# Kernel optimization log

Measured on AMD Instinct MI355X. Metric: run time of the kernel, lower is better.

The kernel has to match this reference:

```python
import jax, jax.numpy as jnp
import numpy as np

NUM_HEADS = 16  # matches init_kwargs; used only for the softmax scale


def setup_inputs() -> dict:
    key = jax.random.key(0)
    ks = jax.random.split(key, 6)
    B, S, H = 2, 4096, 2048
    W_STD = 0.02  # keep pre-softmax logits in a sane range
    return {
        "hidden_states": jax.random.normal(ks[0], (B, S, H), dtype=jnp.float32),
        "freqs_angle": jax.random.uniform(ks[1], (H // 2,), dtype=jnp.float32),
        "wq": jax.random.normal(ks[2], (H, H), dtype=jnp.float32) * W_STD,
        "wk": jax.random.normal(ks[3], (H, H), dtype=jnp.float32) * W_STD,
        "wv": jax.random.normal(ks[4], (H, H), dtype=jnp.float32) * W_STD,
        "wo": jax.random.normal(ks[5], (H, H), dtype=jnp.float32) * W_STD,
        "num_heads": NUM_HEADS,
    }


def _apply_rotary(x, cos, sin):
    # x: [B,S,H]; split full hidden dim into (real, imag) halves of size d=H//2,
    # complex-multiply by exp(i*theta) (theta shape [d], broadcast over B,S),
    # then emit torch.view_as_real's INTERLEAVED layout [re0, im0, re1, im1, ...].
    d = x.shape[-1] // 2
    xr, xi = x[..., :d], x[..., d:]
    out_r = xr * cos - xi * sin
    out_i = xr * sin + xi * cos
    return jnp.stack([out_r, out_i], axis=-1).reshape(x.shape)  # [B,S,2d]


def reference(hidden_states, freqs_angle, wq, wk, wv, wo, num_heads):
    H = hidden_states.shape[-1]
    scale = 1.0 / float(np.sqrt(H // num_heads))

    q = jnp.einsum("bsh,oh->bso", hidden_states, wq)
    k = jnp.einsum("bsh,oh->bso", hidden_states, wk)
    v = jnp.einsum("bsh,oh->bso", hidden_states, wv)

    cos, sin = jnp.cos(freqs_angle), jnp.sin(freqs_angle)
    q_rot = _apply_rotary(q, cos, sin)
    k_rot = _apply_rotary(k, cos, sin)

    # full-hidden-dim attention (module never reshapes into heads)
    scores = jnp.einsum("bqh,bkh->bqk", q_rot, k_rot) * scale  # [B,S,S]
    probs = jax.nn.softmax(scores, axis=-1)
    out = jnp.einsum("bqk,bkh->bqh", probs, v)
    return jnp.einsum("bsh,oh->bso", out, wo)
```

## Files before the change

### kernel.cpp

```cpp
#include <hip/hip_runtime.h>
#include <hip/hip_fp16.h>


typedef _Float16 half8 __attribute__((ext_vector_type(8)));
typedef _Float16 half4v __attribute__((ext_vector_type(4)));
typedef float f32x4 __attribute__((ext_vector_type(4)));

using gas_t = const __attribute__((address_space(1))) void;
using las_t = __attribute__((address_space(3))) void;
#define GL2LDS16(g, l) __builtin_amdgcn_global_load_lds((gas_t*)(g), (las_t*)(l), 16, 0, 0)

#define BAR() __builtin_amdgcn_s_barrier()
#define VMW(N) asm volatile("s_waitcnt vmcnt(" #N ")" ::: "memory")


#define FRAGS(BUF, KS, QC)                                                        \
  half8 af[8], bf[2];                                                             \
  _Pragma("unroll") for (int mi = 0; mi < 8; ++mi)                                \
      af[mi] = *(const half8*)&lds[(BUF)*32768 + (KS)*8192 + aoff + mi*512];      \
  _Pragma("unroll") for (int ni = 0; ni < 2; ++ni)                                \
      bf[ni] = *(const half8*)&lds[(BUF)*32768 + 16384 + (KS)*8192 + boff + (QC)*1024 + ni*512];

#define MFMA8x2(QC)                                                               \
  __builtin_amdgcn_s_setprio(1);                                                  \
  _Pragma("unroll") for (int mi = 0; mi < 8; ++mi) {                              \
    acc[mi][(QC)*2+0] = __builtin_amdgcn_mfma_f32_16x16x32_f16(af[mi], bf[0], acc[mi][(QC)*2+0], 0, 0, 0); \
    acc[mi][(QC)*2+1] = __builtin_amdgcn_mfma_f32_16x16x32_f16(af[mi], bf[1], acc[mi][(QC)*2+1], 0, 0, 0); \
  }                                                                               \
  __builtin_amdgcn_s_setprio(0);

#define STAGE(GP, LD, RB, KT, KS, BUFI, ISB)                                      \
  {                                                                               \
    const _Float16* _s = (GP) + (size_t)((RB) + srow) * (LD) + (KT) + (KS)*32 + scl*8; \
    _Float16* _d = lds + (BUFI)*32768 + (ISB)*16384 + (KS)*8192 + wv*512 + lane*8;     \
    GL2LDS16(_s, _d);                                                             \
    GL2LDS16(_s + (size_t)128*(LD), _d + 4096);                                   \
  }

template <typename OutT>
__global__ __launch_bounds__(512, 2) void gemm256(
    const _Float16* __restrict__ A, const _Float16* __restrict__ B,
    OutT* __restrict__ C, int K, int lda, int ldb, int ldc,
    size_t saz, size_t sbz, size_t scz) {
  extern __shared__ __align__(16) _Float16 lds[];

  const int tid = threadIdx.x;
  const int lane = tid & 63;
  const int wv = tid >> 6;
  const int wr = wv >> 2;
  const int wcol = wv & 3;
  const int r16 = lane & 15, kq = lane >> 4;
  const int chk = kq ^ ((r16 >> 1) & 3);
  const int aoff = (wr * 128 + r16) * 32 + chk * 8;
  const int boff = (wcol * 64 + r16) * 32 + chk * 8;
  const int srow = (wv << 4) + (lane >> 2);
  const int scl = (lane & 3) ^ ((lane >> 3) & 3);

  const int gx = gridDim.x, gy = gridDim.y;
  const int nwg = gx * gy * (int)gridDim.z;
  const int flat = blockIdx.x + gx * (blockIdx.y + gy * blockIdx.z);
  const int swz = (flat & 7) * (nwg >> 3) + (flat >> 3);
  const int tn = swz % gx;
  const int rem = swz / gx;
  const int tm = rem % gy;
  const int bz = rem / gy;
  const _Float16* Ab = A + (size_t)bz * saz;
  const _Float16* Bb = B + (size_t)bz * sbz;
  OutT* Cb = C + (size_t)bz * scz;
  const int mBase = tm * 256, nBase = tn * 256;

  f32x4 acc[8][4] = {};

  STAGE(Ab, lda, mBase, 0, 0, 0, 0);
  STAGE(Bb, ldb, nBase, 0, 0, 0, 1);
  STAGE(Ab, lda, mBase, 0, 1, 0, 0);
  STAGE(Bb, ldb, nBase, 0, 1, 0, 1);
  STAGE(Ab, lda, mBase, 64, 0, 1, 0);
  STAGE(Bb, ldb, nBase, 64, 0, 1, 1);
  VMW(4);
  BAR();

  const int NIT = K >> 7;
  for (int it = 0; it < NIT - 1; ++it) {
    const int kt1 = it * 128 + 64, kt2 = it * 128 + 128, kt3 = it * 128 + 192;
    { FRAGS(0,0,0); STAGE(Ab, lda, mBase, kt1, 1, 1, 0); BAR(); MFMA8x2(0); BAR(); }
    { FRAGS(0,0,1); STAGE(Bb, ldb, nBase, kt1, 1, 1, 1); BAR(); MFMA8x2(1); VMW(8); BAR(); }
    { FRAGS(0,1,0); STAGE(Ab, lda, mBase, kt2, 0, 0, 0); BAR(); MFMA8x2(0); BAR(); }
    { FRAGS(0,1,1); STAGE(Bb, ldb, nBase, kt2, 0, 0, 1); BAR(); MFMA8x2(1); VMW(8); BAR(); }
    { FRAGS(1,0,0); STAGE(Ab, lda, mBase, kt2, 1, 0, 0); BAR(); MFMA8x2(0); BAR(); }
    { FRAGS(1,0,1); STAGE(Bb, ldb, nBase, kt2, 1, 0, 1); BAR(); MFMA8x2(1); VMW(8); BAR(); }
    { FRAGS(1,1,0); STAGE(Ab, lda, mBase, kt3, 0, 1, 0); BAR(); MFMA8x2(0); BAR(); }
    { FRAGS(1,1,1); STAGE(Bb, ldb, nBase, kt3, 0, 1, 1); BAR(); MFMA8x2(1); VMW(8); BAR(); }
  }
  const int ktL = K - 64;
  { FRAGS(0,0,0); STAGE(Ab, lda, mBase, ktL, 1, 1, 0); BAR(); MFMA8x2(0); BAR(); }
  { FRAGS(0,0,1); STAGE(Bb, ldb, nBase, ktL, 1, 1, 1); BAR(); MFMA8x2(1); VMW(8); BAR(); }
  { FRAGS(0,1,0); BAR(); MFMA8x2(0); BAR(); }
  { FRAGS(0,1,1); BAR(); MFMA8x2(1); VMW(4); BAR(); }
  { FRAGS(1,0,0); BAR(); MFMA8x2(0); BAR(); }
  { FRAGS(1,0,1); BAR(); MFMA8x2(1); VMW(0); BAR(); }
  { FRAGS(1,1,0); BAR(); MFMA8x2(0); BAR(); }
  { FRAGS(1,1,1); BAR(); MFMA8x2(1); }

  const size_t crow0 = (size_t)mBase + wr * 128 + kq * 4;
  const size_t ccol = (size_t)nBase + wcol * 64 + r16;
#pragma unroll
  for (int mi = 0; mi < 8; ++mi)
#pragma unroll
    for (int n = 0; n < 4; ++n)
#pragma unroll
      for (int r = 0; r < 4; ++r)
        Cb[(crow0 + mi * 16 + r) * (size_t)ldc + ccol + n * 16] = (OutT)acc[mi][n][r];
}

__global__ __launch_bounds__(256) void prep(
    const float* __restrict__ hid, const float* __restrict__ ang,
    const float* __restrict__ wq, const float* __restrict__ wk,
    const float* __restrict__ wv, const float* __restrict__ wo,
    _Float16* __restrict__ Xh, _Float16* __restrict__ WqR,
    _Float16* __restrict__ WkR, _Float16* __restrict__ Wvh,
    _Float16* __restrict__ Woh) {
  const int z = blockIdx.z;
  const int start = blockIdx.x * 256 + threadIdx.x;
  const int stride = gridDim.x * 256;
  if (z <= 1) {
    const float* w = z ? wk : wq;
    _Float16* o = z ? WkR : WqR;
    const float sc = z ? 1.0f : 0.08838834764831845f;
    for (int u = start; u < 1024 * 512; u += stride) {
      const int i = u >> 9;
      const int c = (u & 511) << 2;
      const float a = ang[i];
      const float cv = cosf(a) * sc, sv = sinf(a) * sc;
      f32x4 ar = *(const f32x4*)&w[(size_t)i * 2048 + c];
      f32x4 br = *(const f32x4*)&w[(size_t)(i + 1024) * 2048 + c];
      half4v r0, r1;
#pragma unroll
      for (int j = 0; j < 4; ++j) {
        r0[j] = (_Float16)(ar[j] * cv - br[j] * sv);
        r1[j] = (_Float16)(ar[j] * sv + br[j] * cv);
      }
      *(half4v*)&o[(size_t)(2 * i) * 2048 + c] = r0;
      *(half4v*)&o[(size_t)(2 * i + 1) * 2048 + c] = r1;
    }
  } else if (z <= 3) {
    const float* w = (z == 2) ? wv : wo;
    _Float16* o = (z == 2) ? Wvh : Woh;
    for (int u = start; u < 2048 * 512; u += stride) {
      const int c = u << 2;
      f32x4 a = *(const f32x4*)&w[c];
      half4v r;
#pragma unroll
      for (int j = 0; j < 4; ++j) r[j] = (_Float16)a[j];
      *(half4v*)&o[c] = r;
    }
  } else {
    for (int u = start; u < (2 * 4096 * 2048) / 4; u += stride) {
      const int c = u << 2;
      f32x4 a = *(const f32x4*)&hid[c];
      half4v r;
#pragma unroll
      for (int j = 0; j < 4; ++j) r[j] = (_Float16)a[j];
      *(half4v*)&Xh[c] = r;
    }
  }
}

__global__ __launch_bounds__(256) void softmax_rows(_Float16* __restrict__ Sm) {
  _Float16* p = Sm + (size_t)blockIdx.x * 4096;
  const int tid = threadIdx.x;
  const int lane = tid & 63, wave = tid >> 6;
  __shared__ float red[8];

  half8 v0 = *(const half8*)&p[tid * 16];
  half8 v1 = *(const half8*)&p[tid * 16 + 8];
  float x[16];
#pragma unroll
  for (int j = 0; j < 8; ++j) { x[j] = (float)v0[j]; x[8 + j] = (float)v1[j]; }

  float m = x[0];
#pragma unroll
  for (int j = 1; j < 16; ++j) m = fmaxf(m, x[j]);
#pragma unroll
  for (int msk = 32; msk >= 1; msk >>= 1) m = fmaxf(m, __shfl_xor(m, msk));
  if (lane == 0) red[wave] = m;
  __syncthreads();
  m = fmaxf(fmaxf(red[0], red[1]), fmaxf(red[2], red[3]));

  float s = 0.f;
#pragma unroll
  for (int j = 0; j < 16; ++j) { x[j] = __expf(x[j] - m); s += x[j]; }
#pragma unroll
  for (int msk = 32; msk >= 1; msk >>= 1) s += __shfl_xor(s, msk);
  if (lane == 0) red[4 + wave] = s;
  __syncthreads();
  s = red[4] + red[5] + red[6] + red[7];
  const float inv = 1.0f / s;

#pragma unroll
  for (int j = 0; j < 8; ++j) {
    v0[j] = (_Float16)(x[j] * inv);
    v1[j] = (_Float16)(x[8 + j] * inv);
  }
  *(half8*)&p[tid * 16] = v0;
  *(half8*)&p[tid * 16 + 8] = v1;
}

extern "C" void kernel_launch(void* const* d_in, const int* in_sizes, int n_in,
                              void* d_out, int out_size, void* d_ws, size_t ws_size,
                              hipStream_t stream) {
  (void)in_sizes; (void)n_in; (void)out_size; (void)ws_size;
  const float* hid = (const float*)d_in[0];
  const float* ang = (const float*)d_in[1];
  const float* wq  = (const float*)d_in[2];
  const float* wk  = (const float*)d_in[3];
  const float* wv  = (const float*)d_in[4];
  const float* wo  = (const float*)d_in[5];
  float* out = (float*)d_out;

  _Float16* ws = (_Float16*)d_ws;
  const size_t EX = 2ull * 4096 * 2048;
  const size_t EH = 2048ull * 2048;
  _Float16* Xh  = ws;
  _Float16* AO  = ws;
  _Float16* Q   = ws + EX;
  _Float16* Kh  = ws + 2 * EX;
  _Float16* Vt  = ws + 3 * EX;
  _Float16* WqR = ws + 4 * EX;
  _Float16* WkR = WqR + EH;
  _Float16* Wvh = WkR + EH;
  _Float16* Woh = Wvh + EH;
  _Float16* Sm  = Woh + EH;

  (void)hipFuncSetAttribute((const void*)&gemm256<_Float16>,
                            hipFuncAttributeMaxDynamicSharedMemorySize, 131072);
  (void)hipFuncSetAttribute((const void*)&gemm256<float>,
                            hipFuncAttributeMaxDynamicSharedMemorySize, 131072);

  prep<<<dim3(2048, 1, 5), 256, 0, stream>>>(hid, ang, wq, wk, wv, wo, Xh, WqR, WkR, Wvh, Woh);

  gemm256<_Float16><<<dim3(8, 32, 2), 512, 131072, stream>>>(
      Xh, WqR, Q, 2048, 2048, 2048, 2048, 0, EH, EX);

  gemm256<_Float16><<<dim3(16, 8, 2), 512, 131072, stream>>>(
      Wvh, Xh, Vt, 2048, 2048, 2048, 4096, 0, (size_t)4096 * 2048, (size_t)2048 * 4096);

  gemm256<_Float16><<<dim3(16, 16, 2), 512, 131072, stream>>>(
      Q, Kh, Sm, 2048, 2048, 2048, 4096, (size_t)4096 * 2048, (size_t)4096 * 2048,
      (size_t)4096 * 4096);

  softmax_rows<<<8192, 256, 0, stream>>>(Sm);

  gemm256<_Float16><<<dim3(8, 16, 2), 512, 131072, stream>>>(
      Sm, Vt, AO, 4096, 4096, 4096, 2048, (size_t)4096 * 4096, (size_t)2048 * 4096,
      (size_t)4096 * 2048);

  gemm256<float><<<dim3(8, 32, 1), 512, 131072, stream>>>(
      AO, Woh, out, 2048, 2048, 2048, 2048, 0, 0, 0);
}
```

Before: 712.1 us.

## Double-buffer MFMA register fragments to overlap LDS reads with matrix math

```diff
diff --git a/kernel.cpp b/kernel.cpp
--- a/kernel.cpp
+++ b/kernel.cpp
@@ -14,18 +14,19 @@
 #define VMW(N) asm volatile("s_waitcnt vmcnt(" #N ")" ::: "memory")
 
 
-#define FRAGS(BUF, KS, QC)                                                        \
-  half8 af[8], bf[2];                                                             \
+#define LDA8(DST, BUF, KS)                                                        \
   _Pragma("unroll") for (int mi = 0; mi < 8; ++mi)                                \
-      af[mi] = *(const half8*)&lds[(BUF)*32768 + (KS)*8192 + aoff + mi*512];      \
+      DST[mi] = *(const half8*)&lds[(BUF)*32768 + (KS)*8192 + aoff + mi*512];
+
+#define LDB2(DST, BUF, KS, QC)                                                    \
   _Pragma("unroll") for (int ni = 0; ni < 2; ++ni)                                \
-      bf[ni] = *(const half8*)&lds[(BUF)*32768 + 16384 + (KS)*8192 + boff + (QC)*1024 + ni*512];
-
-#define MFMA8x2(QC)                                                               \
+      DST[ni] = *(const half8*)&lds[(BUF)*32768 + 16384 + (KS)*8192 + boff + (QC)*1024 + ni*512];
+
+#define MFMA8x2(AF, BF, QC)                                                       \
   __builtin_amdgcn_s_setprio(1);                                                  \
   _Pragma("unroll") for (int mi = 0; mi < 8; ++mi) {                              \
-    acc[mi][(QC)*2+0] = __builtin_amdgcn_mfma_f32_16x16x32_f16(af[mi], bf[0], acc[mi][(QC)*2+0], 0, 0, 0); \
-    acc[mi][(QC)*2+1] = __builtin_amdgcn_mfma_f32_16x16x32_f16(af[mi], bf[1], acc[mi][(QC)*2+1], 0, 0, 0); \
+    acc[mi][(QC)*2+0] = __builtin_amdgcn_mfma_f32_16x16x32_f16(AF[mi], BF[0], acc[mi][(QC)*2+0], 0, 0, 0); \
+    acc[mi][(QC)*2+1] = __builtin_amdgcn_mfma_f32_16x16x32_f16(AF[mi], BF[1], acc[mi][(QC)*2+1], 0, 0, 0); \
   }                                                                               \
   __builtin_amdgcn_s_setprio(0);
 
@@ -70,6 +71,9 @@
   const int mBase = tm * 256, nBase = tn * 256;
 
   f32x4 acc[8][4] = {};
+  half8 afA[8], afB[8];
+  half8 bfA0[2], bfA1[2];
+  half8 bfB0[2], bfB1[2];
 
   STAGE(Ab, lda, mBase, 0, 0, 0, 0);
   STAGE(Bb, ldb, nBase, 0, 0, 0, 1);
@@ -79,28 +83,30 @@
   STAGE(Bb, ldb, nBase, 64, 0, 1, 1);
   VMW(4);
   BAR();
+  LDA8(afA, 0, 0);
+  LDB2(bfA0, 0, 0, 0);
 
   const int NIT = K >> 7;
   for (int it = 0; it < NIT - 1; ++it) {
     const int kt1 = it * 128 + 64, kt2 = it * 128 + 128, kt3 = it * 128 + 192;
-    { FRAGS(0,0,0); STAGE(Ab, lda, mBase, kt1, 1, 1, 0); BAR(); MFMA8x2(0); BAR(); }
-    { FRAGS(0,0,1); STAGE(Bb, ldb, nBase, kt1, 1, 1, 1); BAR(); MFMA8x2(1); VMW(8); BAR(); }
-    { FRAGS(0,1,0); STAGE(Ab, lda, mBase, kt2, 0, 0, 0); BAR(); MFMA8x2(0); BAR(); }
-    { FRAGS(0,1,1); STAGE(Bb, ldb, nBase, kt2, 0, 0, 1); BAR(); MFMA8x2(1); VMW(8); BAR(); }
-    { FRAGS(1,0,0); STAGE(Ab, lda, mBase, kt2, 1, 0, 0); BAR(); MFMA8x2(0); BAR(); }
-    { FRAGS(1,0,1); STAGE(Bb, ldb, nBase, kt2, 1, 0, 1); BAR(); MFMA8x2(1); VMW(8); BAR(); }
-    { FRAGS(1,1,0); STAGE(Ab, lda, mBase, kt3, 0, 1, 0); BAR(); MFMA8x2(0); BAR(); }
-    { FRAGS(1,1,1); STAGE(Bb, ldb, nBase, kt3, 0, 1, 1); BAR(); MFMA8x2(1); VMW(8); BAR(); }
+    { STAGE(Ab, lda, mBase, kt1, 1, 1, 0); BAR(); LDB2(bfA1, 0, 0, 1);                    MFMA8x2(afA, bfA0, 0); VMW(6); BAR(); }
+    { STAGE(Bb, ldb, nBase, kt1, 1, 1, 1); BAR(); LDA8(afB, 0, 1); LDB2(bfB0, 0, 1, 0);   MFMA8x2(afA, bfA1, 1);         BAR(); }
+    { STAGE(Ab, lda, mBase, kt2, 0, 0, 0); BAR(); LDB2(bfB1, 0, 1, 1);                    MFMA8x2(afB, bfB0, 0); VMW(6); BAR(); }
+    { STAGE(Bb, ldb, nBase, kt2, 0, 0, 1); BAR(); LDA8(afA, 1, 0); LDB2(bfA0, 1, 0, 0);   MFMA8x2(afB, bfB1, 1);         BAR(); }
+    { STAGE(Ab, lda, mBase, kt2, 1, 0, 0); BAR(); LDB2(bfA1, 1, 0, 1);                    MFMA8x2(afA, bfA0, 0); VMW(6); BAR(); }
+    { STAGE(Bb, ldb, nBase, kt2, 1, 0, 1); BAR(); LDA8(afB, 1, 1); LDB2(bfB0, 1, 1, 0);   MFMA8x2(afA, bfA1, 1);         BAR(); }
+    { STAGE(Ab, lda, mBase, kt3, 0, 1, 0); BAR(); LDB2(bfB1, 1, 1, 1);                    MFMA8x2(afB, bfB0, 0); VMW(6); BAR(); }
+    { STAGE(Bb, ldb, nBase, kt3, 0, 1, 1); BAR(); LDA8(afA, 0, 0); LDB2(bfA0, 0, 0, 0);   MFMA8x2(afB, bfB1, 1);         BAR(); }
   }
   const int ktL = K - 64;
-  { FRAGS(0,0,0); STAGE(Ab, lda, mBase, ktL, 1, 1, 0); BAR(); MFMA8x2(0); BAR(); }
-  { FRAGS(0,0,1); STAGE(Bb, ldb, nBase, ktL, 1, 1, 1); BAR(); MFMA8x2(1); VMW(8); BAR(); }
-  { FRAGS(0,1,0); BAR(); MFMA8x2(0); BAR(); }
-  { FRAGS(0,1,1); BAR(); MFMA8x2(1); VMW(4); BAR(); }
-  { FRAGS(1,0,0); BAR(); MFMA8x2(0); BAR(); }
-  { FRAGS(1,0,1); BAR(); MFMA8x2(1); VMW(0); BAR(); }
-  { FRAGS(1,1,0); BAR(); MFMA8x2(0); BAR(); }
-  { FRAGS(1,1,1); BAR(); MFMA8x2(1); }
+  { STAGE(Ab, lda, mBase, ktL, 1, 1, 0); BAR(); LDB2(bfA1, 0, 0, 1);                    MFMA8x2(afA, bfA0, 0); VMW(6); BAR(); }
+  { STAGE(Bb, ldb, nBase, ktL, 1, 1, 1); BAR(); LDA8(afB, 0, 1); LDB2(bfB0, 0, 1, 0);   MFMA8x2(afA, bfA1, 1);         BAR(); }
+  {                                      BAR(); LDB2(bfB1, 0, 1, 1);                    MFMA8x2(afB, bfB0, 0); VMW(4); BAR(); }
+  {                                      BAR(); LDA8(afA, 1, 0); LDB2(bfA0, 1, 0, 0);   MFMA8x2(afB, bfB1, 1);         BAR(); }
+  {                                      BAR(); LDB2(bfA1, 1, 0, 1);                    MFMA8x2(afA, bfA0, 0); VMW(0); BAR(); }
+  {                                      BAR(); LDA8(afB, 1, 1); LDB2(bfB0, 1, 1, 0);   MFMA8x2(afA, bfA1, 1);         BAR(); }
+  {                                      BAR(); LDB2(bfB1, 1, 1, 1);                    MFMA8x2(afB, bfB0, 0);         BAR(); }
+  {                                                                                     MFMA8x2(afB, bfB1, 1);                }
 
   const size_t crow0 = (size_t)mBase + wr * 128 + kq * 4;
   const size_t ccol = (size_t)nBase + wcol * 64 + r16;
```

Measured after the change: 793.4 us. +11.4%, slower.
